# Kernel tuning notes

Hardware: AMD Instinct MI355X
Metric: run time of the kernel (lower is better)

## Reference

```python
import jax, jax.numpy as jnp
import numpy as np
import math

D_MODEL = 1024
N_HEADS = 16
QKV_DIM = 1024
D_HEAD = QKV_DIM // N_HEADS


def setup_inputs() -> dict:
    key = jax.random.key(0)
    ks = jax.random.split(key, 10)
    B, S = 4, 2048
    lim = 1.0 / math.sqrt(D_MODEL)
    lim_o = 1.0 / math.sqrt(QKV_DIM)
    return {
        "x": jax.random.normal(ks[0], (B, S, D_MODEL), dtype=jnp.float32),
        "w_q": jax.random.uniform(ks[1], (QKV_DIM, D_MODEL), minval=-lim, maxval=lim, dtype=jnp.float32),
        "b_q": jax.random.uniform(ks[2], (QKV_DIM,), minval=-lim, maxval=lim, dtype=jnp.float32),
        "w_k": jax.random.uniform(ks[3], (QKV_DIM, D_MODEL), minval=-lim, maxval=lim, dtype=jnp.float32),
        "b_k": jax.random.uniform(ks[4], (QKV_DIM,), minval=-lim, maxval=lim, dtype=jnp.float32),
        "w_v": jax.random.uniform(ks[5], (QKV_DIM, D_MODEL), minval=-lim, maxval=lim, dtype=jnp.float32),
        "b_v": jax.random.uniform(ks[6], (QKV_DIM,), minval=-lim, maxval=lim, dtype=jnp.float32),
        "w_o": jax.random.uniform(ks[7], (D_MODEL, QKV_DIM), minval=-lim_o, maxval=lim_o, dtype=jnp.float32),
        "b_o": jax.random.uniform(ks[8], (D_MODEL,), minval=-lim_o, maxval=lim_o, dtype=jnp.float32),
        "temperature": jnp.ones((1,), dtype=jnp.float32),
        "q_scale": jnp.ones((N_HEADS,), dtype=jnp.float32),
    }


def reference(x, w_q, b_q, w_k, b_k, w_v, b_v, w_o, b_o, temperature, q_scale):
    B, S, _ = x.shape
    # QKV projections: [B,S,qkv_dim] -> [B,H,S,Dh]
    def proj(w, b):
        y = jnp.einsum('bsd,ed->bse', x, w) + b
        return y.reshape(B, S, N_HEADS, D_HEAD).transpose(0, 2, 1, 3)
    q = proj(w_q, b_q)
    k = proj(w_k, b_k)
    v = proj(w_v, b_v)
    scale = jnp.sqrt(jnp.float32(D_HEAD)) * temperature[0]
    scores = jnp.einsum('bhqd,bhkd->bhqk', q, k) / scale
    attn = jax.nn.softmax(scores, axis=-1)
    attn = attn * q_scale.reshape(1, N_HEADS, 1, 1)  # per-head post-softmax scale
    out = jnp.einsum('bhqk,bhkd->bhqd', attn, v)
    out = out.transpose(0, 2, 1, 3).reshape(B, S, QKV_DIM)
    return jnp.einsum('bse,de->bsd', out, w_o) + b_o
```

## Files before the change

### kernel.cpp

```cpp
#include <hip/hip_runtime.h>
#include <hip/hip_bf16.h>
#include <stdint.h>

typedef __bf16 bf16;
typedef __bf16 bf16x8 __attribute__((ext_vector_type(8)));
typedef __bf16 bf16x4 __attribute__((ext_vector_type(4)));
typedef float f32x4 __attribute__((ext_vector_type(4)));
typedef float f32x16 __attribute__((ext_vector_type(16)));

#define NB 4
#define SEQ 2048
#define DM 1024
#define NHEADS 16
#define DHEAD 64
#define MTOK (NB*SEQ)
#define NE 3072

__device__ __forceinline__ void gl_lds16(const bf16* g, bf16* l) {
  __builtin_amdgcn_global_load_lds(
      (const __attribute__((address_space(1))) void*)g,
      (__attribute__((address_space(3))) void*)l, 16, 0, 0);
}

__device__ __forceinline__ f32x16 zero16() {
  f32x16 z;
#pragma unroll
  for (int i=0;i<16;i++) z[i]=0.f;
  return z;
}

__global__ __launch_bounds__(256) void convert_kernel(
    const float* __restrict__ x,
    const float* __restrict__ wq, const float* __restrict__ wk,
    const float* __restrict__ wv, const float* __restrict__ wo,
    const float* __restrict__ bq, const float* __restrict__ bk,
    const float* __restrict__ bv,
    bf16* __restrict__ xb, bf16* __restrict__ wqkvb,
    bf16* __restrict__ wob, float* __restrict__ bqkv) {
  int tid = blockIdx.x*blockDim.x + threadIdx.x;
  int nt = gridDim.x*blockDim.x;
  const int NX4 = MTOK*DM/4;
  for (int i = tid; i < NX4; i += nt) {
    float4 v = ((const float4*)x)[i];
    ((bf16x4*)xb)[i] = bf16x4{(bf16)v.x,(bf16)v.y,(bf16)v.z,(bf16)v.w};
  }
  const int NW4 = DM*DM/4;
  for (int i = tid; i < NW4; i += nt) {
    float4 a = ((const float4*)wq)[i];
    ((bf16x4*)wqkvb)[i] = bf16x4{(bf16)a.x,(bf16)a.y,(bf16)a.z,(bf16)a.w};
    float4 b = ((const float4*)wk)[i];
    ((bf16x4*)wqkvb)[i+NW4] = bf16x4{(bf16)b.x,(bf16)b.y,(bf16)b.z,(bf16)b.w};
    float4 c = ((const float4*)wv)[i];
    ((bf16x4*)wqkvb)[i+2*NW4] = bf16x4{(bf16)c.x,(bf16)c.y,(bf16)c.z,(bf16)c.w};
    float4 d = ((const float4*)wo)[i];
    ((bf16x4*)wob)[i] = bf16x4{(bf16)d.x,(bf16)d.y,(bf16)d.z,(bf16)d.w};
  }
  for (int i = tid; i < DM; i += nt) {
    bqkv[i] = bq[i]; bqkv[i+DM] = bk[i]; bqkv[i+2*DM] = bv[i];
  }
}

template<int OUT_MODE>
__global__ __launch_bounds__(256) void gemm_deep(
    const bf16* __restrict__ A, const bf16* __restrict__ Bm,
    const float* __restrict__ bias, void* __restrict__ Cout,
    int M, int N, int K) {
  __shared__ bf16 As[2][128*64];
  __shared__ bf16 Bs[2][128*64];
  const int bm = blockIdx.x, bn = blockIdx.y;
  const int thr = threadIdx.x;
  const int w = thr>>6, lane = thr&63;
  const int wr = w>>1, wc = w&1;
  const int l4 = lane>>4, lm = lane&15;
  f32x4 acc[4][4];
#pragma unroll
  for (int m=0;m<4;m++)
#pragma unroll
    for (int n=0;n<4;n++) acc[m][n] = f32x4{0.f,0.f,0.f,0.f};

  const bf16* Abase = A + (size_t)bm*128*K;
  const bf16* Bbase = Bm + (size_t)bn*128*K;

  const int srow = thr>>3;
  const int sch  = ((thr&7) ^ (srow&7)) * 8;
  const bf16* Ag = Abase + (size_t)srow*K + sch;
  const bf16* Bg = Bbase + (size_t)srow*K + sch;
  const int dbase = thr*8;

  const int nk = K>>6;

  int aoff[2][4], boff[2][4];
#pragma unroll
  for (int ks=0;ks<2;ks++) {
#pragma unroll
    for (int m=0;m<4;m++) {
      const int r = wr*64 + m*16 + lm;
      aoff[ks][m] = r*64 + ((((ks<<2)|l4) ^ (lm&7))*8);
    }
#pragma unroll
    for (int n=0;n<4;n++) {
      const int r = wc*64 + n*16 + lm;
      boff[ks][n] = r*64 + ((((ks<<2)|l4) ^ (lm&7))*8);
    }
  }

#pragma unroll
  for (int c=0;c<4;c++) {
    gl_lds16(Ag + (size_t)c*32*K, &As[0][c*2048 + dbase]);
    gl_lds16(Bg + (size_t)c*32*K, &Bs[0][c*2048 + dbase]);
  }

  for (int kt=0; kt<nk; ++kt) {
    const int p = kt&1;
    const int st = (kt+1 < nk) ? kt+1 : 0;
    const size_t ko = (size_t)st*64;
#pragma unroll
    for (int c=0;c<4;c++) {
      gl_lds16(Ag + ko + (size_t)c*32*K, &As[p^1][c*2048 + dbase]);
      gl_lds16(Bg + ko + (size_t)c*32*K, &Bs[p^1][c*2048 + dbase]);
    }
    asm volatile("s_waitcnt vmcnt(8)" ::: "memory");
    __builtin_amdgcn_s_barrier();
    __builtin_amdgcn_sched_barrier(0);

    const bf16* Ac = As[p];
    const bf16* Bc = Bs[p];
    __builtin_amdgcn_s_setprio(1);
#pragma unroll
    for (int ks=0;ks<2;ks++) {
      bf16x8 af[4], bfr[4];
#pragma unroll
      for (int m=0;m<4;m++) af[m] = *(const bf16x8*)&Ac[aoff[ks][m]];
#pragma unroll
      for (int n=0;n<4;n++) bfr[n] = *(const bf16x8*)&Bc[boff[ks][n]];
#pragma unroll
      for (int m=0;m<4;m++)
#pragma unroll
        for (int n=0;n<4;n++)
          acc[m][n] = __builtin_amdgcn_mfma_f32_16x16x32_bf16(af[m], bfr[n], acc[m][n], 0, 0, 0);
    }
    __builtin_amdgcn_s_setprio(0);
    __builtin_amdgcn_s_barrier();
    __builtin_amdgcn_sched_barrier(0);
  }

  const int rbase = bm*128 + wr*64 + l4*4;
  const int cbase = bn*128 + wc*64;
#pragma unroll
  for (int n=0;n<4;n++) {
    const int col = cbase + n*16 + lm;
    const float bv = bias[col];
#pragma unroll
    for (int m=0;m<4;m++) {
#pragma unroll
      for (int j=0;j<4;j++) {
        const int row = rbase + m*16 + j;
        const float v = acc[m][n][j] + bv;
        if (OUT_MODE == 0) ((bf16*)Cout)[(size_t)row*N + col] = (bf16)v;
        else               ((float*)Cout)[(size_t)row*N + col] = v;
      }
    }
  }
}

__global__ __launch_bounds__(256) void transpose_v(const bf16* __restrict__ qkv,
                                                   bf16* __restrict__ vt) {
  __shared__ bf16 tile[64*72];
  const int s0 = blockIdx.x*64;
  const int bh = blockIdx.y;
  const bf16* src = qkv + (size_t)((bh>>4)*SEQ + s0)*NE + 2*DM + (bh&15)*64;
  const int thr = threadIdx.x;
#pragma unroll
  for (int i=0;i<2;i++) {
    int idx = thr + i*256;
    int row = idx>>3, part = idx&7;
    *(bf16x8*)&tile[row*72 + part*8] = *(const bf16x8*)(src + (size_t)row*NE + part*8);
  }
  __syncthreads();
  bf16* dst = vt + (size_t)bh*64*SEQ + s0;
#pragma unroll
  for (int i=0;i<2;i++) {
    int idx = thr + i*256;
    int d = idx>>3, part = idx&7;
    bf16x8 v;
#pragma unroll
    for (int j=0;j<8;j++) v[j] = tile[(part*8+j)*72 + d];
    *(bf16x8*)(dst + (size_t)d*SEQ + part*8) = v;
  }
}

__global__ __launch_bounds__(256) void attn_kernel(
    const bf16* __restrict__ qkv, const bf16* __restrict__ vt,
    bf16* __restrict__ aout,
    const float* __restrict__ temperature, const float* __restrict__ q_scale) {
  __shared__ bf16 Ks[2][64*64];
  __shared__ bf16 Vs[2][64*64];
  const int bh = blockIdx.y;
  const int b = bh>>4, h = bh&15;
  const int thr = threadIdx.x;
  const int w = thr>>6, lane = thr&63;
  const int l31 = lane&31, hi = lane>>5;
  const float sc2 = 1.4426950408889634f / (8.0f * temperature[0]);
  const int q0 = blockIdx.x*128 + w*32;

  bf16x8 qf[4];
  {
    const bf16* qp = qkv + (size_t)(b*SEQ + q0 + l31)*NE + h*64 + hi*8;
#pragma unroll
    for (int s=0;s<4;s++) qf[s] = *(const bf16x8*)(qp + s*16);
  }

  float l_run = 0.f;
  f32x16 o0 = zero16(), o1 = zero16();

  const bf16* Kbase = qkv + (size_t)b*SEQ*NE + DM + h*64;
  const bf16* Vbase = vt + (size_t)bh*64*SEQ;

  const int sr = thr>>2, scb = thr&3;
  const int wb0 = sr*128 + (((scb*2+0) ^ (sr&7))<<4);
  const int wb1 = sr*128 + (((scb*2+1) ^ (sr&7))<<4);
  const int rsw = l31&7;

  const bf16* kgb = Kbase + (size_t)sr*NE + scb*16;
  const bf16* vgb = Vbase + (size_t)sr*SEQ + scb*16;

  bf16x8 ka, kb, va, vb;
  ka = *(const bf16x8*)(kgb);
  kb = *(const bf16x8*)(kgb + 8);
  va = *(const bf16x8*)(vgb);
  vb = *(const bf16x8*)(vgb + 8);
  *(bf16x8*)((char*)Ks[0] + wb0) = ka;
  *(bf16x8*)((char*)Ks[0] + wb1) = kb;
  *(bf16x8*)((char*)Vs[0] + wb0) = va;
  *(bf16x8*)((char*)Vs[0] + wb1) = vb;
  ka = *(const bf16x8*)(kgb + (size_t)64*NE);
  kb = *(const bf16x8*)(kgb + (size_t)64*NE + 8);
  va = *(const bf16x8*)(vgb + 64);
  vb = *(const bf16x8*)(vgb + 64 + 8);
  __syncthreads();

  for (int t=0; t<SEQ/64; ++t) {
    const int p = t&1;
    const bf16* Kc = Ks[p];
    const bf16* Vc = Vs[p];
    if (t < SEQ/64-1) {
      *(bf16x8*)((char*)Ks[p^1] + wb0) = ka;
      *(bf16x8*)((char*)Ks[p^1] + wb1) = kb;
      *(bf16x8*)((char*)Vs[p^1] + wb0) = va;
      *(bf16x8*)((char*)Vs[p^1] + wb1) = vb;
      if (t < SEQ/64-2) {
        const size_t ko = (size_t)(t+2)*64;
        ka = *(const bf16x8*)(kgb + ko*NE);
        kb = *(const bf16x8*)(kgb + ko*NE + 8);
        va = *(const bf16x8*)(vgb + ko);
        vb = *(const bf16x8*)(vgb + ko + 8);
      }
    }

    f32x16 st0 = zero16(), st1 = zero16();
    __builtin_amdgcn_s_setprio(1);
#pragma unroll
    for (int s=0;s<4;s++) {
      const int slot = s*2 + hi;
      bf16x8 kf0 = *(const bf16x8*)((const char*)Kc + l31*128 + ((slot ^ rsw)<<4));
      bf16x8 kf1 = *(const bf16x8*)((const char*)Kc + (32+l31)*128 + ((slot ^ rsw)<<4));
      st0 = __builtin_amdgcn_mfma_f32_32x32x16_bf16(kf0, qf[s], st0, 0, 0, 0);
      st1 = __builtin_amdgcn_mfma_f32_32x32x16_bf16(kf1, qf[s], st1, 0, 0, 0);
    }
    __builtin_amdgcn_s_setprio(0);

    float rs = 0.f;
#pragma unroll
    for (int r=0;r<16;r++) {
      st0[r] = __builtin_amdgcn_exp2f(st0[r]*sc2);
      rs += st0[r];
    }
#pragma unroll
    for (int r=0;r<16;r++) {
      st1[r] = __builtin_amdgcn_exp2f(st1[r]*sc2);
      rs += st1[r];
    }
    rs += __shfl_xor(rs, 32);
    l_run += rs;

    __builtin_amdgcn_s_setprio(1);
#pragma unroll
    for (int ks=0;ks<4;ks++) {
      float e0,e1,e2,e3,e4,e5,e6,e7;
      if (ks==0)      { e0=st0[0]; e1=st0[1]; e2=st0[2]; e3=st0[3]; e4=st0[4]; e5=st0[5]; e6=st0[6]; e7=st0[7]; }
      else if (ks==1) { e0=st0[8]; e1=st0[9]; e2=st0[10];e3=st0[11];e4=st0[12];e5=st0[13];e6=st0[14];e7=st0[15]; }
      else if (ks==2) { e0=st1[0]; e1=st1[1]; e2=st1[2]; e3=st1[3]; e4=st1[4]; e5=st1[5]; e6=st1[6]; e7=st1[7]; }
      else            { e0=st1[8]; e1=st1[9]; e2=st1[10];e3=st1[11];e4=st1[12];e5=st1[13];e6=st1[14];e7=st1[15]; }
      unsigned a0,a1,b0,b1;
      asm("v_cvt_pk_bf16_f32 %0, %1, %2" : "=v"(a0) : "v"(e0), "v"(e1));
      asm("v_cvt_pk_bf16_f32 %0, %1, %2" : "=v"(a1) : "v"(e2), "v"(e3));
      asm("v_cvt_pk_bf16_f32 %0, %1, %2" : "=v"(b0) : "v"(e4), "v"(e5));
      asm("v_cvt_pk_bf16_f32 %0, %1, %2" : "=v"(b1) : "v"(e6), "v"(e7));
      asm("v_permlane32_swap_b32 %0, %1" : "+v"(a0), "+v"(b0));
      asm("v_permlane32_swap_b32 %0, %1" : "+v"(a1), "+v"(b1));
      union { unsigned u[4]; bf16x8 v; } pu;
      pu.u[0]=a0; pu.u[1]=a1; pu.u[2]=b0; pu.u[3]=b1;
      const int slot = ks*2 + hi;
      bf16x8 vf0 = *(const bf16x8*)((const char*)Vc + l31*128 + ((slot ^ rsw)<<4));
      bf16x8 vf1 = *(const bf16x8*)((const char*)Vc + (32+l31)*128 + ((slot ^ rsw)<<4));
      o0 = __builtin_amdgcn_mfma_f32_32x32x16_bf16(pu.v, vf0, o0, 0, 0, 0);
      o1 = __builtin_amdgcn_mfma_f32_32x32x16_bf16(pu.v, vf1, o1, 0, 0, 0);
    }
    __builtin_amdgcn_s_setprio(0);
    __syncthreads();
  }

  const float inv = q_scale[h] / l_run;
#pragma unroll
  for (int r=0;r<16;r++) {
    const int qi = (r&3) + 8*(r>>2) + hi*4;
    float iv = __shfl(inv, qi);
    bf16* op = aout + (size_t)(b*SEQ + q0 + qi)*DM + h*64 + l31;
    op[0]  = (bf16)(o0[r]*iv);
    op[32] = (bf16)(o1[r]*iv);
  }
}

extern "C" void kernel_launch(void* const* d_in, const int* in_sizes, int n_in,
                              void* d_out, int out_size, void* d_ws, size_t ws_size,
                              hipStream_t stream) {
  (void)in_sizes; (void)n_in; (void)out_size; (void)ws_size;
  const float* x  = (const float*)d_in[0];
  const float* wq = (const float*)d_in[1];
  const float* bq = (const float*)d_in[2];
  const float* wk = (const float*)d_in[3];
  const float* bk = (const float*)d_in[4];
  const float* wv = (const float*)d_in[5];
  const float* bv = (const float*)d_in[6];
  const float* wo = (const float*)d_in[7];
  const float* bo = (const float*)d_in[8];
  const float* temp = (const float*)d_in[9];
  const float* qsc  = (const float*)d_in[10];

  char* ws = (char*)d_ws;
  bf16* xb    = (bf16*)ws; ws += (size_t)MTOK*DM*2;
  bf16* wqkvb = (bf16*)ws; ws += (size_t)NE*DM*2;
  bf16* wob   = (bf16*)ws; ws += (size_t)DM*DM*2;
  float* bqkv = (float*)ws; ws += (size_t)NE*4;
  bf16* qkv   = (bf16*)ws; ws += (size_t)MTOK*NE*2;
  bf16* vt    = (bf16*)ws; ws += (size_t)NB*NHEADS*DHEAD*SEQ*2;
  bf16* aout  = (bf16*)ws; ws += (size_t)MTOK*DM*2;

  convert_kernel<<<dim3(1024), dim3(256), 0, stream>>>(x, wq, wk, wv, wo, bq, bk, bv,
                                                       xb, wqkvb, wob, bqkv);
  gemm_deep<0><<<dim3(MTOK/128, NE/128), dim3(256), 0, stream>>>(xb, wqkvb, bqkv, qkv,
                                                                 MTOK, NE, DM);
  transpose_v<<<dim3(SEQ/64, NB*NHEADS), dim3(256), 0, stream>>>(qkv, vt);
  attn_kernel<<<dim3(SEQ/128, NB*NHEADS), dim3(256), 0, stream>>>(qkv, vt, aout, temp, qsc);
  gemm_deep<1><<<dim3(MTOK/128, DM/128), dim3(256), 0, stream>>>(aout, wob, bo, d_out,
                                                                 MTOK, DM, DM);
}
```

Measured before the change: 202.0 us.

## Pad attention LDS rows, prescale Q, unroll tile loop by two

Replaces the XOR-swizzled K/V shared-memory layout with padded rows (136-byte stride) and compile-time buffer offsets. The loop is unrolled by two so the double-buffer index becomes constant. The softmax scale is folded into Q once at load time, removing a multiply per score. The row-sum cross-lane shuffle is deferred to after the loop. Prescaling Q in bf16 adds rounding error, and the padded stride may bring back LDS bank conflicts.

```diff
diff --git a/kernel.cpp b/kernel.cpp
--- a/kernel.cpp
+++ b/kernel.cpp
@@ -189,12 +189,16 @@
   }
 }
 
+#define KROW 136
+#define KBUF (64*KROW)
+#define VOFF (2*KBUF)
+
 __global__ __launch_bounds__(256) void attn_kernel(
     const bf16* __restrict__ qkv, const bf16* __restrict__ vt,
     bf16* __restrict__ aout,
     const float* __restrict__ temperature, const float* __restrict__ q_scale) {
-  __shared__ bf16 Ks[2][64*64];
-  __shared__ bf16 Vs[2][64*64];
+  __shared__ bf16 smem[4*64*68];
+  char* lds = (char*)smem;
   const int bh = blockIdx.y;
   const int b = bh>>4, h = bh&15;
   const int thr = threadIdx.x;
@@ -202,24 +206,28 @@
   const int l31 = lane&31, hi = lane>>5;
   const float sc2 = 1.4426950408889634f / (8.0f * temperature[0]);
   const int q0 = blockIdx.x*128 + w*32;
+  const int NT = SEQ/64;
 
   bf16x8 qf[4];
   {
     const bf16* qp = qkv + (size_t)(b*SEQ + q0 + l31)*NE + h*64 + hi*8;
 #pragma unroll
-    for (int s=0;s<4;s++) qf[s] = *(const bf16x8*)(qp + s*16);
-  }
-
-  float l_run = 0.f;
+    for (int s=0;s<4;s++) {
+      bf16x8 qr = *(const bf16x8*)(qp + s*16);
+#pragma unroll
+      for (int j=0;j<8;j++) qf[s][j] = (bf16)((float)qr[j] * sc2);
+    }
+  }
+
+  float l_part = 0.f;
   f32x16 o0 = zero16(), o1 = zero16();
 
   const bf16* Kbase = qkv + (size_t)b*SEQ*NE + DM + h*64;
   const bf16* Vbase = vt + (size_t)bh*64*SEQ;
 
   const int sr = thr>>2, scb = thr&3;
-  const int wb0 = sr*128 + (((scb*2+0) ^ (sr&7))<<4);
-  const int wb1 = sr*128 + (((scb*2+1) ^ (sr&7))<<4);
-  const int rsw = l31&7;
+  const int wbase = sr*KROW + scb*32;
+  const int rbase = l31*KROW + hi*16;
 
   const bf16* kgb = Kbase + (size_t)sr*NE + scb*16;
   const bf16* vgb = Vbase + (size_t)sr*SEQ + scb*16;
@@ -229,87 +237,89 @@
   kb = *(const bf16x8*)(kgb + 8);
   va = *(const bf16x8*)(vgb);
   vb = *(const bf16x8*)(vgb + 8);
-  *(bf16x8*)((char*)Ks[0] + wb0) = ka;
-  *(bf16x8*)((char*)Ks[0] + wb1) = kb;
-  *(bf16x8*)((char*)Vs[0] + wb0) = va;
-  *(bf16x8*)((char*)Vs[0] + wb1) = vb;
+  *(bf16x8*)(lds + wbase)             = ka;
+  *(bf16x8*)(lds + wbase + 16)        = kb;
+  *(bf16x8*)(lds + VOFF + wbase)      = va;
+  *(bf16x8*)(lds + VOFF + wbase + 16) = vb;
   ka = *(const bf16x8*)(kgb + (size_t)64*NE);
   kb = *(const bf16x8*)(kgb + (size_t)64*NE + 8);
   va = *(const bf16x8*)(vgb + 64);
   vb = *(const bf16x8*)(vgb + 64 + 8);
   __syncthreads();
 
-  for (int t=0; t<SEQ/64; ++t) {
-    const int p = t&1;
-    const bf16* Kc = Ks[p];
-    const bf16* Vc = Vs[p];
-    if (t < SEQ/64-1) {
-      *(bf16x8*)((char*)Ks[p^1] + wb0) = ka;
-      *(bf16x8*)((char*)Ks[p^1] + wb1) = kb;
-      *(bf16x8*)((char*)Vs[p^1] + wb0) = va;
-      *(bf16x8*)((char*)Vs[p^1] + wb1) = vb;
-      if (t < SEQ/64-2) {
-        const size_t ko = (size_t)(t+2)*64;
-        ka = *(const bf16x8*)(kgb + ko*NE);
-        kb = *(const bf16x8*)(kgb + ko*NE + 8);
-        va = *(const bf16x8*)(vgb + ko);
-        vb = *(const bf16x8*)(vgb + ko + 8);
-      }
-    }
-
-    f32x16 st0 = zero16(), st1 = zero16();
-    __builtin_amdgcn_s_setprio(1);
-#pragma unroll
-    for (int s=0;s<4;s++) {
-      const int slot = s*2 + hi;
-      bf16x8 kf0 = *(const bf16x8*)((const char*)Kc + l31*128 + ((slot ^ rsw)<<4));
-      bf16x8 kf1 = *(const bf16x8*)((const char*)Kc + (32+l31)*128 + ((slot ^ rsw)<<4));
-      st0 = __builtin_amdgcn_mfma_f32_32x32x16_bf16(kf0, qf[s], st0, 0, 0, 0);
-      st1 = __builtin_amdgcn_mfma_f32_32x32x16_bf16(kf1, qf[s], st1, 0, 0, 0);
-    }
-    __builtin_amdgcn_s_setprio(0);
-
-    float rs = 0.f;
-#pragma unroll
-    for (int r=0;r<16;r++) {
-      st0[r] = __builtin_amdgcn_exp2f(st0[r]*sc2);
-      rs += st0[r];
-    }
-#pragma unroll
-    for (int r=0;r<16;r++) {
-      st1[r] = __builtin_amdgcn_exp2f(st1[r]*sc2);
-      rs += st1[r];
-    }
-    rs += __shfl_xor(rs, 32);
-    l_run += rs;
-
-    __builtin_amdgcn_s_setprio(1);
-#pragma unroll
-    for (int ks=0;ks<4;ks++) {
-      float e0,e1,e2,e3,e4,e5,e6,e7;
-      if (ks==0)      { e0=st0[0]; e1=st0[1]; e2=st0[2]; e3=st0[3]; e4=st0[4]; e5=st0[5]; e6=st0[6]; e7=st0[7]; }
-      else if (ks==1) { e0=st0[8]; e1=st0[9]; e2=st0[10];e3=st0[11];e4=st0[12];e5=st0[13];e6=st0[14];e7=st0[15]; }
-      else if (ks==2) { e0=st1[0]; e1=st1[1]; e2=st1[2]; e3=st1[3]; e4=st1[4]; e5=st1[5]; e6=st1[6]; e7=st1[7]; }
-      else            { e0=st1[8]; e1=st1[9]; e2=st1[10];e3=st1[11];e4=st1[12];e5=st1[13];e6=st1[14];e7=st1[15]; }
-      unsigned a0,a1,b0,b1;
-      asm("v_cvt_pk_bf16_f32 %0, %1, %2" : "=v"(a0) : "v"(e0), "v"(e1));
-      asm("v_cvt_pk_bf16_f32 %0, %1, %2" : "=v"(a1) : "v"(e2), "v"(e3));
-      asm("v_cvt_pk_bf16_f32 %0, %1, %2" : "=v"(b0) : "v"(e4), "v"(e5));
-      asm("v_cvt_pk_bf16_f32 %0, %1, %2" : "=v"(b1) : "v"(e6), "v"(e7));
-      asm("v_permlane32_swap_b32 %0, %1" : "+v"(a0), "+v"(b0));
-      asm("v_permlane32_swap_b32 %0, %1" : "+v"(a1), "+v"(b1));
-      union { unsigned u[4]; bf16x8 v; } pu;
-      pu.u[0]=a0; pu.u[1]=a1; pu.u[2]=b0; pu.u[3]=b1;
-      const int slot = ks*2 + hi;
-      bf16x8 vf0 = *(const bf16x8*)((const char*)Vc + l31*128 + ((slot ^ rsw)<<4));
-      bf16x8 vf1 = *(const bf16x8*)((const char*)Vc + (32+l31)*128 + ((slot ^ rsw)<<4));
-      o0 = __builtin_amdgcn_mfma_f32_32x32x16_bf16(pu.v, vf0, o0, 0, 0, 0);
-      o1 = __builtin_amdgcn_mfma_f32_32x32x16_bf16(pu.v, vf1, o1, 0, 0, 0);
-    }
-    __builtin_amdgcn_s_setprio(0);
-    __syncthreads();
-  }
-
+#define ATTN_TILE(P, T)                                                        \
+  {                                                                            \
+    const int t_ = (T);                                                        \
+    if (t_ < NT-1) {                                                           \
+      *(bf16x8*)(lds + ((P)^1)*KBUF + wbase)             = ka;                 \
+      *(bf16x8*)(lds + ((P)^1)*KBUF + wbase + 16)        = kb;                 \
+      *(bf16x8*)(lds + VOFF + ((P)^1)*KBUF + wbase)      = va;                 \
+      *(bf16x8*)(lds + VOFF + ((P)^1)*KBUF + wbase + 16) = vb;                 \
+      if (t_ < NT-2) {                                                         \
+        const size_t ko_ = (size_t)(t_+2)*64;                                  \
+        ka = *(const bf16x8*)(kgb + ko_*NE);                                   \
+        kb = *(const bf16x8*)(kgb + ko_*NE + 8);                               \
+        va = *(const bf16x8*)(vgb + ko_);                                      \
+        vb = *(const bf16x8*)(vgb + ko_ + 8);                                  \
+      }                                                                        \
+    }                                                                          \
+    f32x16 st0 = zero16(), st1 = zero16();                                     \
+    __builtin_amdgcn_s_setprio(1);                                             \
+    _Pragma("unroll")                                                          \
+    for (int s=0;s<4;s++) {                                                    \
+      bf16x8 kf0 = *(const bf16x8*)(lds + (P)*KBUF + rbase + s*32);            \
+      bf16x8 kf1 = *(const bf16x8*)(lds + (P)*KBUF + rbase + 32*KROW + s*32);  \
+      st0 = __builtin_amdgcn_mfma_f32_32x32x16_bf16(kf0, qf[s], st0, 0,0,0);   \
+      st1 = __builtin_amdgcn_mfma_f32_32x32x16_bf16(kf1, qf[s], st1, 0,0,0);   \
+    }                                                                          \
+    __builtin_amdgcn_s_setprio(0);                                             \
+    _Pragma("unroll")                                                          \
+    for (int r=0;r<16;r++) {                                                   \
+      st0[r] = __builtin_amdgcn_exp2f(st0[r]);                                 \
+      l_part += st0[r];                                                        \
+    }                                                                          \
+    _Pragma("unroll")                                                          \
+    for (int r=0;r<16;r++) {                                                   \
+      st1[r] = __builtin_amdgcn_exp2f(st1[r]);                                 \
+      l_part += st1[r];                                                        \
+    }                                                                          \
+    __builtin_amdgcn_s_setprio(1);                                             \
+    _Pragma("unroll")                                                          \
+    for (int ks=0;ks<4;ks++) {                                                 \
+      float e0,e1,e2,e3,e4,e5,e6,e7;                                           \
+      if (ks==0)      { e0=st0[0]; e1=st0[1]; e2=st0[2]; e3=st0[3];            \
+                        e4=st0[4]; e5=st0[5]; e6=st0[6]; e7=st0[7]; }          \
+      else if (ks==1) { e0=st0[8]; e1=st0[9]; e2=st0[10];e3=st0[11];           \
+                        e4=st0[12];e5=st0[13];e6=st0[14];e7=st0[15]; }         \
+      else if (ks==2) { e0=st1[0]; e1=st1[1]; e2=st1[2]; e3=st1[3];            \
+                        e4=st1[4]; e5=st1[5]; e6=st1[6]; e7=st1[7]; }          \
+      else            { e0=st1[8]; e1=st1[9]; e2=st1[10];e3=st1[11];           \
+                        e4=st1[12];e5=st1[13];e6=st1[14];e7=st1[15]; }         \
+      unsigned a0,a1,b0,b1;                                                    \
+      asm("v_cvt_pk_bf16_f32 %0, %1, %2" : "=v"(a0) : "v"(e0), "v"(e1));       \
+      asm("v_cvt_pk_bf16_f32 %0, %1, %2" : "=v"(a1) : "v"(e2), "v"(e3));       \
+      asm("v_cvt_pk_bf16_f32 %0, %1, %2" : "=v"(b0) : "v"(e4), "v"(e5));       \
+      asm("v_cvt_pk_bf16_f32 %0, %1, %2" : "=v"(b1) : "v"(e6), "v"(e7));       \
+      asm("v_permlane32_swap_b32 %0, %1" : "+v"(a0), "+v"(b0));                \
+      asm("v_permlane32_swap_b32 %0, %1" : "+v"(a1), "+v"(b1));                \
+      union { unsigned u[4]; bf16x8 v; } pu;                                   \
+      pu.u[0]=a0; pu.u[1]=a1; pu.u[2]=b0; pu.u[3]=b1;                          \
+      bf16x8 vf0 = *(const bf16x8*)(lds + VOFF + (P)*KBUF + rbase + ks*32);    \
+      bf16x8 vf1 = *(const bf16x8*)(lds + VOFF + (P)*KBUF + rbase + 32*KROW + ks*32); \
+      o0 = __builtin_amdgcn_mfma_f32_32x32x16_bf16(pu.v, vf0, o0, 0,0,0);      \
+      o1 = __builtin_amdgcn_mfma_f32_32x32x16_bf16(pu.v, vf1, o1, 0,0,0);      \
+    }                                                                          \
+    __builtin_amdgcn_s_setprio(0);                                             \
+    __syncthreads();                                                           \
+  }
+
+  for (int t2=0; t2<NT/2; ++t2) {
+    ATTN_TILE(0, 2*t2);
+    ATTN_TILE(1, 2*t2+1);
+  }
+#undef ATTN_TILE
+
+  float l_run = l_part + __shfl_xor(l_part, 32);
   const float inv = q_scale[h] / l_run;
 #pragma unroll
   for (int r=0;r<16;r++) {
```

Result: slower. 388.0 us (+92.1%).

## Restructure attention: split keys across warps, register-load K/V, MFMA row sums

Applied to the files above, without the earlier changes.

The attention kernel is reorganised so each warp handles 64 queries over half of the key range. K and V fragments are loaded straight from global memory into registers instead of through shared-memory double buffering, which removes the per-tile __syncthreads. The two key halves are combined through shared memory at the end. Row sums come from an extra MFMA against a ones vector, the softmax scale is folded into Q, and the grid is flattened with a block swizzle for L2 locality. In exchange there are more MFMAs, higher register pressure under launch_bounds(256,2), and more global-load latency per key tile.

```diff
diff --git a/kernel.cpp b/kernel.cpp
--- a/kernel.cpp
+++ b/kernel.cpp
@@ -189,135 +189,177 @@
   }
 }
 
-__global__ __launch_bounds__(256) void attn_kernel(
+__global__ __launch_bounds__(256, 2) void attn_kernel(
     const bf16* __restrict__ qkv, const bf16* __restrict__ vt,
     bf16* __restrict__ aout,
     const float* __restrict__ temperature, const float* __restrict__ q_scale) {
-  __shared__ bf16 Ks[2][64*64];
-  __shared__ bf16 Vs[2][64*64];
-  const int bh = blockIdx.y;
-  const int b = bh>>4, h = bh&15;
+  __shared__ float cmb[2][64][96];
+  const int bid = blockIdx.x;
+  const int swz = (bid & 7)*128 + (bid >> 3);
+  const int bh = swz >> 4;
+  const int qb = swz & 15;
+  const int b = bh >> 4, h = bh & 15;
   const int thr = threadIdx.x;
-  const int w = thr>>6, lane = thr&63;
-  const int l31 = lane&31, hi = lane>>5;
+  const int w = thr >> 6, lane = thr & 63;
+  const int qg = w >> 1, kh = w & 1;
+  const int l31 = lane & 31, hi = lane >> 5;
   const float sc2 = 1.4426950408889634f / (8.0f * temperature[0]);
-  const int q0 = blockIdx.x*128 + w*32;
-
-  bf16x8 qf[4];
+  const int q0 = qb*128 + qg*64;
+  const int NTW = SEQ/64/2;
+
+  bf16x8 qfA[4], qfB[4];
   {
-    const bf16* qp = qkv + (size_t)(b*SEQ + q0 + l31)*NE + h*64 + hi*8;
-#pragma unroll
-    for (int s=0;s<4;s++) qf[s] = *(const bf16x8*)(qp + s*16);
-  }
-
-  float l_run = 0.f;
-  f32x16 o0 = zero16(), o1 = zero16();
-
-  const bf16* Kbase = qkv + (size_t)b*SEQ*NE + DM + h*64;
-  const bf16* Vbase = vt + (size_t)bh*64*SEQ;
-
-  const int sr = thr>>2, scb = thr&3;
-  const int wb0 = sr*128 + (((scb*2+0) ^ (sr&7))<<4);
-  const int wb1 = sr*128 + (((scb*2+1) ^ (sr&7))<<4);
-  const int rsw = l31&7;
-
-  const bf16* kgb = Kbase + (size_t)sr*NE + scb*16;
-  const bf16* vgb = Vbase + (size_t)sr*SEQ + scb*16;
-
-  bf16x8 ka, kb, va, vb;
-  ka = *(const bf16x8*)(kgb);
-  kb = *(const bf16x8*)(kgb + 8);
-  va = *(const bf16x8*)(vgb);
-  vb = *(const bf16x8*)(vgb + 8);
-  *(bf16x8*)((char*)Ks[0] + wb0) = ka;
-  *(bf16x8*)((char*)Ks[0] + wb1) = kb;
-  *(bf16x8*)((char*)Vs[0] + wb0) = va;
-  *(bf16x8*)((char*)Vs[0] + wb1) = vb;
-  ka = *(const bf16x8*)(kgb + (size_t)64*NE);
-  kb = *(const bf16x8*)(kgb + (size_t)64*NE + 8);
-  va = *(const bf16x8*)(vgb + 64);
-  vb = *(const bf16x8*)(vgb + 64 + 8);
-  __syncthreads();
-
-  for (int t=0; t<SEQ/64; ++t) {
-    const int p = t&1;
-    const bf16* Kc = Ks[p];
-    const bf16* Vc = Vs[p];
-    if (t < SEQ/64-1) {
-      *(bf16x8*)((char*)Ks[p^1] + wb0) = ka;
-      *(bf16x8*)((char*)Ks[p^1] + wb1) = kb;
-      *(bf16x8*)((char*)Vs[p^1] + wb0) = va;
-      *(bf16x8*)((char*)Vs[p^1] + wb1) = vb;
-      if (t < SEQ/64-2) {
-        const size_t ko = (size_t)(t+2)*64;
-        ka = *(const bf16x8*)(kgb + ko*NE);
-        kb = *(const bf16x8*)(kgb + ko*NE + 8);
-        va = *(const bf16x8*)(vgb + ko);
-        vb = *(const bf16x8*)(vgb + ko + 8);
-      }
-    }
-
-    f32x16 st0 = zero16(), st1 = zero16();
+    const bf16* qpA = qkv + (size_t)(b*SEQ + q0 + l31)*NE + h*64 + hi*8;
+    const bf16* qpB = qpA + (size_t)32*NE;
+#pragma unroll
+    for (int s=0;s<4;s++) {
+      bf16x8 qa = *(const bf16x8*)(qpA + s*16);
+      bf16x8 qb_ = *(const bf16x8*)(qpB + s*16);
+#pragma unroll
+      for (int j=0;j<8;j++) {
+        qfA[s][j] = (bf16)((float)qa[j] * sc2);
+        qfB[s][j] = (bf16)((float)qb_[j] * sc2);
+      }
+    }
+  }
+
+  f32x16 oA0 = zero16(), oA1 = zero16(), lA = zero16();
+  f32x16 oB0 = zero16(), oB1 = zero16(), lB = zero16();
+  const bf16 onev = (bf16)1.0f;
+  const bf16x8 ones = {onev,onev,onev,onev,onev,onev,onev,onev};
+
+  const bf16* kp0 = qkv + (size_t)b*SEQ*NE + DM + h*64
+                  + (size_t)(kh*1024 + l31)*NE + hi*8;
+  const bf16* kp1 = kp0 + (size_t)32*NE;
+  const bf16* vp0 = vt + (size_t)bh*64*SEQ + (size_t)l31*SEQ + kh*1024 + hi*8;
+  const bf16* vp1 = vp0 + (size_t)32*SEQ;
+
+  bf16x8 kf0[4], kf1[4];
+#pragma unroll
+  for (int s=0;s<4;s++) {
+    kf0[s] = *(const bf16x8*)(kp0 + s*16);
+    kf1[s] = *(const bf16x8*)(kp1 + s*16);
+  }
+
+  for (int t=0; t<NTW; ++t) {
+    const int koff = t*64;
+    bf16x8 vf0[4], vf1[4];
+#pragma unroll
+    for (int s=0;s<4;s++) {
+      vf0[s] = *(const bf16x8*)(vp0 + koff + s*16);
+      vf1[s] = *(const bf16x8*)(vp1 + koff + s*16);
+    }
+
+    f32x16 sA0 = zero16(), sA1 = zero16(), sB0 = zero16(), sB1 = zero16();
     __builtin_amdgcn_s_setprio(1);
 #pragma unroll
     for (int s=0;s<4;s++) {
-      const int slot = s*2 + hi;
-      bf16x8 kf0 = *(const bf16x8*)((const char*)Kc + l31*128 + ((slot ^ rsw)<<4));
-      bf16x8 kf1 = *(const bf16x8*)((const char*)Kc + (32+l31)*128 + ((slot ^ rsw)<<4));
-      st0 = __builtin_amdgcn_mfma_f32_32x32x16_bf16(kf0, qf[s], st0, 0, 0, 0);
-      st1 = __builtin_amdgcn_mfma_f32_32x32x16_bf16(kf1, qf[s], st1, 0, 0, 0);
+      sA0 = __builtin_amdgcn_mfma_f32_32x32x16_bf16(kf0[s], qfA[s], sA0, 0,0,0);
+      sB0 = __builtin_amdgcn_mfma_f32_32x32x16_bf16(kf0[s], qfB[s], sB0, 0,0,0);
+      sA1 = __builtin_amdgcn_mfma_f32_32x32x16_bf16(kf1[s], qfA[s], sA1, 0,0,0);
+      sB1 = __builtin_amdgcn_mfma_f32_32x32x16_bf16(kf1[s], qfB[s], sB1, 0,0,0);
     }
     __builtin_amdgcn_s_setprio(0);
 
-    float rs = 0.f;
-#pragma unroll
-    for (int r=0;r<16;r++) {
-      st0[r] = __builtin_amdgcn_exp2f(st0[r]*sc2);
-      rs += st0[r];
-    }
-#pragma unroll
-    for (int r=0;r<16;r++) {
-      st1[r] = __builtin_amdgcn_exp2f(st1[r]*sc2);
-      rs += st1[r];
-    }
-    rs += __shfl_xor(rs, 32);
-    l_run += rs;
+    {
+      const int kn = (t+1 < NTW) ? (t+1)*64 : koff;
+#pragma unroll
+      for (int s=0;s<4;s++) {
+        kf0[s] = *(const bf16x8*)(kp0 + (size_t)kn*NE + s*16);
+        kf1[s] = *(const bf16x8*)(kp1 + (size_t)kn*NE + s*16);
+      }
+    }
+
+#pragma unroll
+    for (int r=0;r<16;r++) sA0[r] = __builtin_amdgcn_exp2f(sA0[r]);
+#pragma unroll
+    for (int r=0;r<16;r++) sA1[r] = __builtin_amdgcn_exp2f(sA1[r]);
+#pragma unroll
+    for (int r=0;r<16;r++) sB0[r] = __builtin_amdgcn_exp2f(sB0[r]);
+#pragma unroll
+    for (int r=0;r<16;r++) sB1[r] = __builtin_amdgcn_exp2f(sB1[r]);
 
     __builtin_amdgcn_s_setprio(1);
 #pragma unroll
     for (int ks=0;ks<4;ks++) {
       float e0,e1,e2,e3,e4,e5,e6,e7;
-      if (ks==0)      { e0=st0[0]; e1=st0[1]; e2=st0[2]; e3=st0[3]; e4=st0[4]; e5=st0[5]; e6=st0[6]; e7=st0[7]; }
-      else if (ks==1) { e0=st0[8]; e1=st0[9]; e2=st0[10];e3=st0[11];e4=st0[12];e5=st0[13];e6=st0[14];e7=st0[15]; }
-      else if (ks==2) { e0=st1[0]; e1=st1[1]; e2=st1[2]; e3=st1[3]; e4=st1[4]; e5=st1[5]; e6=st1[6]; e7=st1[7]; }
-      else            { e0=st1[8]; e1=st1[9]; e2=st1[10];e3=st1[11];e4=st1[12];e5=st1[13];e6=st1[14];e7=st1[15]; }
-      unsigned a0,a1,b0,b1;
+      float f0,f1,f2,f3,f4,f5,f6,f7;
+      if (ks==0)      { e0=sA0[0]; e1=sA0[1]; e2=sA0[2]; e3=sA0[3]; e4=sA0[4]; e5=sA0[5]; e6=sA0[6]; e7=sA0[7];
+                        f0=sB0[0]; f1=sB0[1]; f2=sB0[2]; f3=sB0[3]; f4=sB0[4]; f5=sB0[5]; f6=sB0[6]; f7=sB0[7]; }
+      else if (ks==1) { e0=sA0[8]; e1=sA0[9]; e2=sA0[10];e3=sA0[11];e4=sA0[12];e5=sA0[13];e6=sA0[14];e7=sA0[15];
+                        f0=sB0[8]; f1=sB0[9]; f2=sB0[10];f3=sB0[11];f4=sB0[12];f5=sB0[13];f6=sB0[14];f7=sB0[15]; }
+      else if (ks==2) { e0=sA1[0]; e1=sA1[1]; e2=sA1[2]; e3=sA1[3]; e4=sA1[4]; e5=sA1[5]; e6=sA1[6]; e7=sA1[7];
+                        f0=sB1[0]; f1=sB1[1]; f2=sB1[2]; f3=sB1[3]; f4=sB1[4]; f5=sB1[5]; f6=sB1[6]; f7=sB1[7]; }
+      else            { e0=sA1[8]; e1=sA1[9]; e2=sA1[10];e3=sA1[11];e4=sA1[12];e5=sA1[13];e6=sA1[14];e7=sA1[15];
+                        f0=sB1[8]; f1=sB1[9]; f2=sB1[10];f3=sB1[11];f4=sB1[12];f5=sB1[13];f6=sB1[14];f7=sB1[15]; }
+      unsigned a0,a1,b0,b1,c0,c1,d0,d1;
       asm("v_cvt_pk_bf16_f32 %0, %1, %2" : "=v"(a0) : "v"(e0), "v"(e1));
       asm("v_cvt_pk_bf16_f32 %0, %1, %2" : "=v"(a1) : "v"(e2), "v"(e3));
       asm("v_cvt_pk_bf16_f32 %0, %1, %2" : "=v"(b0) : "v"(e4), "v"(e5));
       asm("v_cvt_pk_bf16_f32 %0, %1, %2" : "=v"(b1) : "v"(e6), "v"(e7));
       asm("v_permlane32_swap_b32 %0, %1" : "+v"(a0), "+v"(b0));
       asm("v_permlane32_swap_b32 %0, %1" : "+v"(a1), "+v"(b1));
-      union { unsigned u[4]; bf16x8 v; } pu;
-      pu.u[0]=a0; pu.u[1]=a1; pu.u[2]=b0; pu.u[3]=b1;
-      const int slot = ks*2 + hi;
-      bf16x8 vf0 = *(const bf16x8*)((const char*)Vc + l31*128 + ((slot ^ rsw)<<4));
-      bf16x8 vf1 = *(const bf16x8*)((const char*)Vc + (32+l31)*128 + ((slot ^ rsw)<<4));
-      o0 = __builtin_amdgcn_mfma_f32_32x32x16_bf16(pu.v, vf0, o0, 0, 0, 0);
-      o1 = __builtin_amdgcn_mfma_f32_32x32x16_bf16(pu.v, vf1, o1, 0, 0, 0);
+      asm("v_cvt_pk_bf16_f32 %0, %1, %2" : "=v"(c0) : "v"(f0), "v"(f1));
+      asm("v_cvt_pk_bf16_f32 %0, %1, %2" : "=v"(c1) : "v"(f2), "v"(f3));
+      asm("v_cvt_pk_bf16_f32 %0, %1, %2" : "=v"(d0) : "v"(f4), "v"(f5));
+      asm("v_cvt_pk_bf16_f32 %0, %1, %2" : "=v"(d1) : "v"(f6), "v"(f7));
+      asm("v_permlane32_swap_b32 %0, %1" : "+v"(c0), "+v"(d0));
+      asm("v_permlane32_swap_b32 %0, %1" : "+v"(c1), "+v"(d1));
+      union { unsigned u[4]; bf16x8 v; } puA, puB;
+      puA.u[0]=a0; puA.u[1]=a1; puA.u[2]=b0; puA.u[3]=b1;
+      puB.u[0]=c0; puB.u[1]=c1; puB.u[2]=d0; puB.u[3]=d1;
+      oA0 = __builtin_amdgcn_mfma_f32_32x32x16_bf16(puA.v, vf0[ks], oA0, 0,0,0);
+      oA1 = __builtin_amdgcn_mfma_f32_32x32x16_bf16(puA.v, vf1[ks], oA1, 0,0,0);
+      lA  = __builtin_amdgcn_mfma_f32_32x32x16_bf16(puA.v, ones, lA, 0,0,0);
+      oB0 = __builtin_amdgcn_mfma_f32_32x32x16_bf16(puB.v, vf0[ks], oB0, 0,0,0);
+      oB1 = __builtin_amdgcn_mfma_f32_32x32x16_bf16(puB.v, vf1[ks], oB1, 0,0,0);
+      lB  = __builtin_amdgcn_mfma_f32_32x32x16_bf16(puB.v, ones, lB, 0,0,0);
     }
     __builtin_amdgcn_s_setprio(0);
-    __syncthreads();
-  }
-
-  const float inv = q_scale[h] / l_run;
-#pragma unroll
-  for (int r=0;r<16;r++) {
-    const int qi = (r&3) + 8*(r>>2) + hi*4;
-    float iv = __shfl(inv, qi);
-    bf16* op = aout + (size_t)(b*SEQ + q0 + qi)*DM + h*64 + l31;
-    op[0]  = (bf16)(o0[r]*iv);
-    op[32] = (bf16)(o1[r]*iv);
+  }
+
+  __syncthreads();
+  if (kh == 1) {
+    float* dst = &cmb[qg][lane][0];
+#pragma unroll
+    for (int r=0;r<16;r++) {
+      dst[r]      = oA0[r];
+      dst[16+r]   = oA1[r];
+      dst[32+r]   = oB0[r];
+      dst[48+r]   = oB1[r];
+      dst[64+r]   = lA[r];
+      dst[80+r]   = lB[r];
+    }
+  }
+  __syncthreads();
+  if (kh == 0) {
+    const float* src = &cmb[qg][lane][0];
+#pragma unroll
+    for (int r=0;r<16;r++) {
+      oA0[r] += src[r];
+      oA1[r] += src[16+r];
+      oB0[r] += src[32+r];
+      oB1[r] += src[48+r];
+      lA[r]  += src[64+r];
+      lB[r]  += src[80+r];
+    }
+    const float qs = q_scale[h];
+#pragma unroll
+    for (int r=0;r<16;r++) {
+      const int qi = (r&3) + 8*(r>>2) + hi*4;
+      {
+        const float iv = qs / lA[r];
+        bf16* op = aout + (size_t)(b*SEQ + q0 + qi)*DM + h*64 + l31;
+        op[0]  = (bf16)(oA0[r]*iv);
+        op[32] = (bf16)(oA1[r]*iv);
+      }
+      {
+        const float iv = qs / lB[r];
+        bf16* op = aout + (size_t)(b*SEQ + q0 + 32 + qi)*DM + h*64 + l31;
+        op[0]  = (bf16)(oB0[r]*iv);
+        op[32] = (bf16)(oB1[r]*iv);
+      }
+    }
   }
 }
 
@@ -351,7 +393,7 @@
   gemm_deep<0><<<dim3(MTOK/128, NE/128), dim3(256), 0, stream>>>(xb, wqkvb, bqkv, qkv,
                                                                  MTOK, NE, DM);
   transpose_v<<<dim3(SEQ/64, NB*NHEADS), dim3(256), 0, stream>>>(qkv, vt);
-  attn_kernel<<<dim3(SEQ/128, NB*NHEADS), dim3(256), 0, stream>>>(qkv, vt, aout, temp, qsc);
+  attn_kernel<<<dim3(1024), dim3(256), 0, stream>>>(qkv, vt, aout, temp, qsc);
   gemm_deep<1><<<dim3(MTOK/128, DM/128), dim3(256), 0, stream>>>(aout, wob, bo, d_out,
                                                                  MTOK, DM, DM);
 }
```

After: 269.4 us. +33.4%, slower.
